# Optimization experiments

Measured on AMD Instinct MI355X. Metric: run time of the kernel, lower is better.

The kernel has to match this reference:

```python
import jax, jax.numpy as jnp
import numpy as np
from jax import lax

EMBED = 512
HID = 512
CLASSES = 3
TP, TH, B = 256, 256, 128
IN_DIM = 768


def _gru_cell(x, h, Wih, Whh, bih, bhh):
    # PyTorch GRU cell math. x: [B, in], h: [B, d]
    gi = x @ Wih.T + bih
    gh = h @ Whh.T + bhh
    i_r, i_z, i_n = jnp.split(gi, 3, axis=-1)
    h_r, h_z, h_n = jnp.split(gh, 3, axis=-1)
    r = jax.nn.sigmoid(i_r + h_r)
    z = jax.nn.sigmoid(i_z + h_z)
    n = jnp.tanh(i_n + r * h_n)
    return (1.0 - z) * n + z * h


def _gru_scan(x, h0, Wih, Whh, bih, bhh):
    # x: [T, B, in]; returns outputs [T, B, d]
    def step(h, xt):
        h = _gru_cell(xt, h, Wih, Whh, bih, bhh)
        return h, h
    _, o = lax.scan(step, h0, x)
    return o


def setup_inputs() -> dict:
    key = jax.random.key(0)
    ks = jax.random.split(key, 32)
    s = 0.02
    d = {
        'encoded_p': jax.random.normal(ks[0], (TP, B, IN_DIM), jnp.float32),
        'encoded_h': jax.random.normal(ks[1], (TH, B, IN_DIM), jnp.float32),
        'p_W': jax.random.normal(ks[2], (EMBED, IN_DIM), jnp.float32) * s,
        'p_b': jnp.zeros((EMBED,), jnp.float32),
        'h_W': jax.random.normal(ks[3], (EMBED, IN_DIM), jnp.float32) * s,
        'h_b': jnp.zeros((EMBED,), jnp.float32),
        'pg_Wih': jax.random.normal(ks[4], (3 * HID, EMBED), jnp.float32) * s,
        'pg_Whh': jax.random.normal(ks[5], (3 * HID, HID), jnp.float32) * s,
        'pg_bih': jnp.zeros((3 * HID,), jnp.float32),
        'pg_bhh': jnp.zeros((3 * HID,), jnp.float32),
        'hg_Wih': jax.random.normal(ks[6], (3 * HID, EMBED), jnp.float32) * s,
        'hg_Whh': jax.random.normal(ks[7], (3 * HID, HID), jnp.float32) * s,
        'hg_bih': jnp.zeros((3 * HID,), jnp.float32),
        'hg_bhh': jnp.zeros((3 * HID,), jnp.float32),
        'W_s': jax.random.normal(ks[8], (HID, HID), jnp.float32) * s,
        'W_t': jax.random.normal(ks[9], (HID, HID), jnp.float32) * s,
        'w_e': jax.random.normal(ks[10], (HID, 1), jnp.float32) * s,
        'W_m': jax.random.normal(ks[11], (HID, HID), jnp.float32) * s,
        'm_Wih': jax.random.normal(ks[12], (3 * HID, 2 * HID), jnp.float32) * s,
        'm_Whh': jax.random.normal(ks[13], (3 * HID, HID), jnp.float32) * s,
        'm_bih': jnp.zeros((3 * HID,), jnp.float32),
        'm_bhh': jnp.zeros((3 * HID,), jnp.float32),
        'out_W': jax.random.normal(ks[14], (CLASSES, HID), jnp.float32) * s,
        'out_b': jnp.zeros((CLASSES,), jnp.float32),
        'training': 0,
    }
    return d


def reference(encoded_p, encoded_h, p_W, p_b, h_W, h_b,
              pg_Wih, pg_Whh, pg_bih, pg_bhh,
              hg_Wih, hg_Whh, hg_bih, hg_bhh,
              W_s, W_t, w_e, W_m,
              m_Wih, m_Whh, m_bih, m_bhh,
              out_W, out_b, training):
    batch = encoded_p.shape[1]
    # dropout is identity when training is falsy (reference uses training=0)
    xp = encoded_p @ p_W.T + p_b          # [Tp, B, embed]
    xh = encoded_h @ h_W.T + h_b          # [Th, B, embed]
    h0 = jnp.ones((batch, HID), xp.dtype)  # torch.ones init hidden
    o_p = _gru_scan(xp, h0, pg_Wih, pg_Whh, pg_bih, pg_bhh)  # [Tp, B, d]
    o_h = _gru_scan(xh, h0, hg_Wih, hg_Whh, hg_bih, hg_bhh)  # [Th, B, d]

    Whs = jnp.einsum('tbd,de->tbe', o_p, W_s)  # precompute, fixed across steps
    we = w_e[:, 0]

    def step(h_m, h_t):
        Wht = h_t @ W_t                        # [B, d]
        Wm = h_m @ W_m                         # [B, d]
        M = jnp.tanh(Whs + (Wht + Wm)[None])   # [Tp, B, d]
        logits = jnp.einsum('tbd,d->bt', M, we)  # [B, Tp]
        alpha = jax.nn.softmax(logits, axis=1)
        a_t = jnp.einsum('bt,tbd->bd', alpha, o_p)
        m_t = jnp.concatenate([a_t, h_t], axis=-1)  # [B, 2d]
        h_m = _gru_cell(m_t, h_m, m_Wih, m_Whh, m_bih, m_bhh)
        return h_m, alpha

    h_m0 = jnp.ones((batch, HID), xp.dtype)
    h_star, _alphas = lax.scan(step, h_m0, o_h)
    out = h_star @ out_W.T + out_b
    out = jax.nn.relu(out)  # LAST_NON_LINEAR = True
    return out
```

## Files before the change

kernel.cpp:

```cpp
#include <hip/hip_runtime.h>
#include <cstddef>

#define TSEQ 256
#define NB   128
#define HID  512
#define G3   1536
#define INDIM 768
#define CH   16
#define NWG  256
#define FLS  32

typedef unsigned short bfraw;
using short8 = __attribute__((ext_vector_type(8))) short;
using f32x4  = __attribute__((ext_vector_type(4))) float;

#define MFMA16 __builtin_amdgcn_mfma_f32_16x16x32_bf16

__device__ __forceinline__ float bf2f(unsigned int u){ return __uint_as_float(u<<16); }
__device__ __forceinline__ bfraw f2bf(float f){
  unsigned int u = __float_as_uint(f);
  u += 0x7fffu + ((u>>16)&1u);
  return (bfraw)(u>>16);
}
__device__ __forceinline__ float fsig(float x){
  return __builtin_amdgcn_rcpf(1.0f + __expf(-x));
}
__device__ __forceinline__ float ftanh(float x){
  return 1.0f - 2.0f*__builtin_amdgcn_rcpf(1.0f + __expf(2.0f*x));
}

__device__ __forceinline__ uint4 bpu4(const void* p){
  unsigned long long a = __hip_atomic_load((const unsigned long long*)p,     __ATOMIC_RELAXED, __HIP_MEMORY_SCOPE_AGENT);
  unsigned long long b = __hip_atomic_load((const unsigned long long*)p + 1, __ATOMIC_RELAXED, __HIP_MEMORY_SCOPE_AGENT);
  uint4 r; r.x=(unsigned)a; r.y=(unsigned)(a>>32); r.z=(unsigned)b; r.w=(unsigned)(b>>32);
  return r;
}
__device__ __forceinline__ short8 bps8(const void* p){
  union{ uint4 u; short8 s; } cv; cv.u = bpu4(p); return cv.s;
}
__device__ __forceinline__ float4 bpf4(const void* p){
  union{ uint4 u; float4 f; } cv; cv.u = bpu4(p); return cv.f;
}
__device__ __forceinline__ float bpf(const void* p){
  unsigned u = __hip_atomic_load((const unsigned*)p, __ATOMIC_RELAXED, __HIP_MEMORY_SCOPE_AGENT);
  return __uint_as_float(u);
}
__device__ __forceinline__ void st4_cp(void* p, unsigned v){
  __hip_atomic_store((unsigned*)p, v, __ATOMIC_RELAXED, __HIP_MEMORY_SCOPE_AGENT);
}
__device__ __forceinline__ void st8_cp(void* p, unsigned long long v){
  __hip_atomic_store((unsigned long long*)p, v, __ATOMIC_RELAXED, __HIP_MEMORY_SCOPE_AGENT);
}
__device__ __forceinline__ void stf_cp(float* p, float v){
  __hip_atomic_store((unsigned*)p, __float_as_uint(v), __ATOMIC_RELAXED, __HIP_MEMORY_SCOPE_AGENT);
}
__device__ __forceinline__ void sth_cp(bfraw* p, bfraw v){
  __hip_atomic_store((unsigned short*)p, v, __ATOMIC_RELAXED, __HIP_MEMORY_SCOPE_AGENT);
}
__device__ __forceinline__ unsigned long long pk64(float a, float b){
  return (unsigned long long)__float_as_uint(a) | ((unsigned long long)__float_as_uint(b)<<32);
}

__device__ __forceinline__ void spin_ge(unsigned* p, unsigned epoch){
  int sp = 0;
  while (__hip_atomic_load(p, __ATOMIC_RELAXED, __HIP_MEMORY_SCOPE_AGENT) < epoch){
    if (sp < 3){ __builtin_amdgcn_s_sleep(1); ++sp; }
    else        __builtin_amdgcn_s_sleep(16);
  }
}
__device__ __forceinline__ void pollN(unsigned* flags, int n, unsigned epoch){
  const int tid = threadIdx.x;
  if (tid < n) spin_ge(&flags[tid*FLS], epoch);
  __syncthreads();
}
__device__ __forceinline__ void setflag(unsigned* f, unsigned v){
  if (threadIdx.x == 0){
    asm volatile("s_waitcnt vmcnt(0)" ::: "memory");
    __hip_atomic_store(f, v, __ATOMIC_RELAXED, __HIP_MEMORY_SCOPE_AGENT);
  }
}

__global__ void init_k(unsigned* bar){
  int i = blockIdx.x*256 + threadIdx.x;
  if (i < 4*NWG*FLS) bar[i] = 0u;
}

__global__ void hminit_k(float* hmbuf, bfraw* hm_bf){
  int i = blockIdx.x*256 + threadIdx.x;
  hmbuf[i] = 1.0f;
  hm_bf[i] = (bfraw)0x3f80;
}

__global__ __launch_bounds__(256)
void tconv_k(const float* __restrict__ in, bfraw* __restrict__ out, int R, int Cc){
  __shared__ float t[32][33];
  int c0 = blockIdx.x*32, r0 = blockIdx.y*32;
  int tx = threadIdx.x&31, ty = threadIdx.x>>5;
  #pragma unroll
  for (int i=0;i<32;i+=8) t[ty+i][tx] = in[(size_t)(r0+ty+i)*Cc + c0+tx];
  __syncthreads();
  #pragma unroll
  for (int i=0;i<32;i+=8) out[(size_t)(c0+ty+i)*R + r0+tx] = f2bf(t[tx][ty+i]);
}

__global__ void cvt_k(const float* __restrict__ in, bfraw* __restrict__ out, int n){
  int i = (blockIdx.x*256 + threadIdx.x)*4;
  if (i >= n) return;
  float4 v = *(const float4*)(in+i);
  uint2 o;
  o.x = (unsigned)f2bf(v.x) | ((unsigned)f2bf(v.y)<<16);
  o.y = (unsigned)f2bf(v.z) | ((unsigned)f2bf(v.w)<<16);
  *(uint2*)(out+i) = o;
}

__global__ void wcat_k(const float* __restrict__ mWih, const float* __restrict__ mWhh,
                       bfraw* __restrict__ Wcat){
  size_t gid = (size_t)blockIdx.x*256 + threadIdx.x;
  int np = (int)(gid / 384);
  int k4 = ((int)(gid % 384))*4;
  int dd = np>>2, g = np&3;
  float v[4];
  #pragma unroll
  for (int j=0;j<4;++j){
    int k = k4+j; float x = 0.f;
    if (g==0)      x = (k<1024) ? mWih[(size_t)dd*1024 + k]        : mWhh[(size_t)dd*512 + (k-1024)];
    else if (g==1) x = (k<1024) ? mWih[(size_t)(512+dd)*1024 + k]  : mWhh[(size_t)(512+dd)*512 + (k-1024)];
    else if (g==2) x = (k<1024) ? mWih[(size_t)(1024+dd)*1024 + k] : 0.f;
    else           x = (k<1024) ? 0.f : mWhh[(size_t)(1024+dd)*512 + (k-1024)];
    v[j] = x;
  }
  uint2 o;
  o.x = (unsigned)f2bf(v[0]) | ((unsigned)f2bf(v[1])<<16);
  o.y = (unsigned)f2bf(v[2]) | ((unsigned)f2bf(v[3])<<16);
  *(uint2*)(Wcat + (size_t)np*1536 + k4) = o;
}

__global__ void bpack_k(const float* __restrict__ mbih, const float* __restrict__ mbhh,
                        float* __restrict__ bc){
  int dd = blockIdx.x*256 + threadIdx.x;
  if (dd >= 512) return;
  bc[dd]      = mbih[dd] + mbhh[dd];
  bc[512+dd]  = mbih[512+dd] + mbhh[512+dd];
  bc[1024+dd] = mbih[1024+dd];
  bc[1536+dd] = mbhh[1024+dd];
}

__global__ void fuse_bias_k(const float* __restrict__ Wih, const float* __restrict__ bih,
                            const float* __restrict__ pb, float* __restrict__ bout)
{
  int g = blockIdx.x*256 + threadIdx.x;
  if (g >= G3) return;
  float acc = bih[g];
  const float* w = Wih + (size_t)g*HID;
  for (int e=0;e<HID;e+=4){
    float4 wv = *(const float4*)(w+e);
    float4 pv = *(const float4*)(pb+e);
    acc += wv.x*pv.x + wv.y*pv.y + wv.z*pv.z + wv.w*pv.w;
  }
  bout[g] = acc;
}

template<typename TA, typename TC, bool BIAS>
__global__ __launch_bounds__(256)
void mgemm(const TA* __restrict__ A0, const TA* __restrict__ A1,
           const bfraw* __restrict__ B0, const bfraw* __restrict__ B1,
           const float* __restrict__ bias0, const float* __restrict__ bias1,
           TC* __restrict__ C0, TC* __restrict__ C1,
           int K, int lda, int ldb, int ldc)
{
  const TA* A = blockIdx.z ? A1 : A0;
  const bfraw* B = blockIdx.z ? B1 : B0;
  const float* bias = blockIdx.z ? bias1 : bias0;
  TC* C = blockIdx.z ? C1 : C0;
  __shared__ bfraw Al[128*40];
  __shared__ bfraw Bl[128*40];
  const int tid = threadIdx.x;
  const size_t m0 = (size_t)blockIdx.y*128, n0 = (size_t)blockIdx.x*128;
  const int w = tid>>6, l = tid&63;
  const int wr = (w>>1)*64, wc = (w&1)*64;
  const int fr = l&15, fg = l>>4;
  f32x4 acc[4][4];
  #pragma unroll
  for (int i=0;i<4;++i)
    #pragma unroll
    for (int j=0;j<4;++j) acc[i][j] = (f32x4){0.f,0.f,0.f,0.f};

  const int srow = tid>>1, skc = (tid&1)*16;
  for (int k0=0; k0<K; k0+=32){
    if constexpr (sizeof(TA)==4){
      const float* ap = (const float*)A + (m0+srow)*lda + k0 + skc;
      float4 v0=*(const float4*)ap, v1=*(const float4*)(ap+4),
             v2=*(const float4*)(ap+8), v3=*(const float4*)(ap+12);
      uint4 w0, w1;
      w0.x=(unsigned)f2bf(v0.x)|((unsigned)f2bf(v0.y)<<16);
      w0.y=(unsigned)f2bf(v0.z)|((unsigned)f2bf(v0.w)<<16);
      w0.z=(unsigned)f2bf(v1.x)|((unsigned)f2bf(v1.y)<<16);
      w0.w=(unsigned)f2bf(v1.z)|((unsigned)f2bf(v1.w)<<16);
      w1.x=(unsigned)f2bf(v2.x)|((unsigned)f2bf(v2.y)<<16);
      w1.y=(unsigned)f2bf(v2.z)|((unsigned)f2bf(v2.w)<<16);
      w1.z=(unsigned)f2bf(v3.x)|((unsigned)f2bf(v3.y)<<16);
      w1.w=(unsigned)f2bf(v3.z)|((unsigned)f2bf(v3.w)<<16);
      *(uint4*)&Al[srow*40+skc]   = w0;
      *(uint4*)&Al[srow*40+skc+8] = w1;
    } else {
      const bfraw* ap = (const bfraw*)A + (m0+srow)*lda + k0 + skc;
      *(uint4*)&Al[srow*40+skc]   = *(const uint4*)ap;
      *(uint4*)&Al[srow*40+skc+8] = *(const uint4*)(ap+8);
    }
    {
      const bfraw* bp = B + (n0+srow)*ldb + k0 + skc;
      *(uint4*)&Bl[srow*40+skc]   = *(const uint4*)bp;
      *(uint4*)&Bl[srow*40+skc+8] = *(const uint4*)(bp+8);
    }
    __syncthreads();
    short8 af[4], bfr[4];
    #pragma unroll
    for (int i=0;i<4;++i) af[i]  = *(const short8*)&Al[(wr+i*16+fr)*40 + fg*8];
    #pragma unroll
    for (int j=0;j<4;++j) bfr[j] = *(const short8*)&Bl[(wc+j*16+fr)*40 + fg*8];
    #pragma unroll
    for (int i=0;i<4;++i)
      #pragma unroll
      for (int j=0;j<4;++j)
        acc[i][j] = MFMA16(af[i], bfr[j], acc[i][j], 0,0,0);
    __syncthreads();
  }
  #pragma unroll
  for (int i=0;i<4;++i){
    #pragma unroll
    for (int j=0;j<4;++j){
      size_t n = n0 + wc + j*16 + fr;
      float bv = BIAS ? bias[n] : 0.f;
      #pragma unroll
      for (int r=0;r<4;++r){
        size_t m = m0 + wr + i*16 + fg*4 + r;
        float v = acc[i][j][r] + bv;
        if constexpr (sizeof(TC)==2) ((bfraw*)C)[m*ldc + n] = f2bf(v);
        else                         ((float*)C)[m*ldc + n] = v;
      }
    }
  }
}

__global__ __launch_bounds__(512, 2)
void scanB(const float* __restrict__ GIp, const float* __restrict__ GIh,
           const bfraw* __restrict__ Whhp, const bfraw* __restrict__ Whhh,
           const float* __restrict__ bhhp, const float* __restrict__ bhhh,
           float* __restrict__ hst, bfraw* __restrict__ o_p, bfraw* __restrict__ o_h,
           int c0, unsigned* __restrict__ bar)
{
  extern __shared__ char smem[];
  bfraw* wl = (bfraw*)smem;
  float* sh = (float*)(smem + 98304);
  const int wg = blockIdx.x;
  const int z = wg>>7, rem = wg&127;
  const int bg = rem>>4, dg = rem&15;
  const float* GI  = z ? GIh : GIp;
  const bfraw* Wb  = z ? Whhh : Whhp;
  const float* bhh = z ? bhhh : bhhp;
  bfraw* ob = z ? o_h : o_p;
  float* hz = hst + (size_t)z*2*NB*HID;
  const int tid = threadIdx.x;
  unsigned* bfl = bar + 3*NWG*FLS;
  unsigned* grp = bfl + (size_t)(z*128 + bg*16)*FLS;
  unsigned* own = bfl + (size_t)wg*FLS;

  #pragma unroll
  for (int g=0; g<3; ++g){
    const unsigned* src = (const unsigned*)(Wb + (size_t)(g*512 + dg*32)*512);
    for (int j=0; j<16; ++j){
      int iu = tid + j*512;
      unsigned v = src[iu];
      int d = iu>>8, kk = (iu&255)*2;
      int idx0 = g*16384 + (kk>>2)*128 + d*4 + (kk&3);
      *((unsigned*)wl + (idx0>>1)) = v;
    }
  }
  __syncthreads();

  const int bl = tid>>5, dl = tid&31;
  const int d = dg*32+dl, bglob = bg*16+bl;
  const float br = bhh[d], bz = bhh[512+d], bn = bhh[1024+d];

  #pragma clang loop unroll(disable)
  for (int tt=0; tt<CH; ++tt){
    const int t = c0+tt;
    if (t > 0) pollN(grp, 16, (unsigned)t);
    if (t == 0){
      for (int j=0;j<4;++j){
        int i4 = tid + j*512;
        *(float4*)&sh[i4*4] = (float4){1.f,1.f,1.f,1.f};
      }
    } else {
      const float* hp = hz + (size_t)((t-1)&1)*NB*HID + (size_t)bg*16*HID;
      for (int j=0;j<4;++j){
        int i4 = tid + j*512;
        *(float4*)&sh[i4*4] = bpf4(&hp[i4*4]);
      }
    }
    __syncthreads();
    float ar = br, az = bz, an = bn;
    const float* hb = sh + bl*512;
    for (int k=0;k<512;k+=4){
      float4 h4 = *(const float4*)(hb+k);
      int base = (k>>2)*128 + dl*4;
      uint2 wr = *(const uint2*)(wl + base);
      uint2 wz = *(const uint2*)(wl + 16384 + base);
      uint2 wn = *(const uint2*)(wl + 32768 + base);
      ar += h4.x*bf2f(wr.x&0xffffu) + h4.y*bf2f(wr.x>>16) + h4.z*bf2f(wr.y&0xffffu) + h4.w*bf2f(wr.y>>16);
      az += h4.x*bf2f(wz.x&0xffffu) + h4.y*bf2f(wz.x>>16) + h4.z*bf2f(wz.y&0xffffu) + h4.w*bf2f(wz.y>>16);
      an += h4.x*bf2f(wn.x&0xffffu) + h4.y*bf2f(wn.x>>16) + h4.z*bf2f(wn.y&0xffffu) + h4.w*bf2f(wn.y>>16);
    }
    const float* gi = GI + ((size_t)tt*NB + bglob)*G3;
    float r  = fsig(gi[d] + ar);
    float zz = fsig(gi[512+d] + az);
    float n  = ftanh(gi[1024+d] + r*an);
    float hp = hb[d];
    float hv = (1.0f-zz)*n + zz*hp;
    stf_cp(&(hz + (size_t)(t&1)*NB*HID)[(size_t)bglob*HID + d], hv);
    ob[((size_t)t*NB + bglob)*HID + d] = f2bf(hv);
    __syncthreads();
    setflag(own, (unsigned)(t+1));
  }
}

__global__ __launch_bounds__(512, 2)
void scanD(const bfraw* __restrict__ Whs, const bfraw* __restrict__ o_p,
           const bfraw* __restrict__ o_h,
           const bfraw* __restrict__ WtT, const bfraw* __restrict__ WmT,
           const float* __restrict__ w_e,
           const bfraw* __restrict__ Wcat, const float* __restrict__ bc,
           float* __restrict__ hmbuf, bfraw* __restrict__ hm_bf,
           bfraw* __restrict__ a_bf, float* __restrict__ Lbuf, float* __restrict__ Gx,
           const float* __restrict__ outW, const float* __restrict__ outb,
           float* __restrict__ out, unsigned* __restrict__ bar)
{
  extern __shared__ char smem[];
  bfraw* whs_l = (bfraw*)smem;
  float* pt    = (float*)(smem + 131072);
  float* xlf   = (float*)(smem + 147456);
  float* hml   = (float*)(smem + 149504);
  float* c_l   = (float*)(smem + 151552);
  float* lp0   = (float*)(smem + 152576);
  float* lp1   = (float*)(smem + 153600);
  float* l_s   = (float*)(smem + 154624);
  float* red   = (float*)(smem + 155648);

  const int wg = blockIdx.x, tid = threadIdx.x;
  const int b = wg>>1, dh = wg&1;
  unsigned* pf  = bar;
  unsigned* afl = bar + NWG*FLS;
  unsigned* hfl = bar + 2*NWG*FLS;

  for (int it=0; it<16; ++it){
    int idx = tid + it*512;
    int tq = idx>>5, c = idx&31;
    const bfraw* src = Whs + ((size_t)tq*NB + b)*HID + dh*256 + c*8;
    *(uint4*)&whs_l[tq*256 + ((c ^ (tq&15))<<3)] = *(const uint4*)src;
  }
  const int cc_ = tid&31;
  float we8[8];
  #pragma unroll
  for (int r=0;r<8;++r) we8[r] = w_e[dh*256 + cc_*8 + r];
  __syncthreads();

  const int gs = wg&127, gbgrp = gs>>4, gddg = gs&15;
  const int gw = tid>>6, gl = tid&63, gfr = gl&15, gfg = gl>>4;
  const int n0w = gddg*128 + gw*16;
  const int mb0 = gbgrp*16;
  const bfraw* wrowA = Wcat + (size_t)(n0w+gfr)*1536;

  #pragma clang loop unroll(disable)
  for (int t=0; t<TSEQ; ++t){
    const int rs = (t+1)&1;
    const bfraw* hmr = hm_bf + (size_t)rs*65536;
    const float* hpr = hmbuf + (size_t)rs*65536;
    bfraw* hmw = hm_bf + (size_t)(t&1)*65536;
    float* hpw = hmbuf + (size_t)(t&1)*65536;

    if (t > 0){
      if (tid < 16) spin_ge(&hfl[((b>>4)*16 + tid)*FLS], (unsigned)t);
      else if (wg < 128 && tid < 32) spin_ge(&hfl[(gbgrp*16 + (tid-16))*FLS], (unsigned)t);
      else if (wg >= 128 && tid == 16) spin_ge(&hfl[gs*FLS], (unsigned)t);
      __syncthreads();
    }

    if (tid < 64){
      uint4 u = *(const uint4*)(o_h + ((size_t)t*NB + b)*HID + tid*8);
      float4 f0, f1;
      f0.x=bf2f(u.x&0xffffu); f0.y=bf2f(u.x>>16); f0.z=bf2f(u.y&0xffffu); f0.w=bf2f(u.y>>16);
      f1.x=bf2f(u.z&0xffffu); f1.y=bf2f(u.z>>16); f1.z=bf2f(u.w&0xffffu); f1.w=bf2f(u.w>>16);
      *(float4*)&xlf[tid*8]   = f0;
      *(float4*)&xlf[tid*8+4] = f1;
    } else if (tid < 192){
      int i2 = tid - 64;
      *(float4*)&hml[i2*4] = bpf4(hpr + (size_t)b*HID + i2*4);
    }
    __syncthreads();

    {
      const int el = tid>>1, kh = tid&1;
      const bfraw* wt = WtT + (size_t)(dh*256+el)*HID + kh*256;
      const bfraw* wm = WmT + (size_t)(dh*256+el)*HID + kh*256;
      const float* xv = xlf + kh*256;
      const float* hv = hml + kh*256;
      float acc = 0.f;
      #pragma unroll 4
      for (int k8=0;k8<32;++k8){
        uint4 wu = *(const uint4*)(wt+k8*8);
        uint4 mu = *(const uint4*)(wm+k8*8);
        float4 x0 = *(const float4*)(xv+k8*8), x1 = *(const float4*)(xv+k8*8+4);
        float4 h0 = *(const float4*)(hv+k8*8), h1 = *(const float4*)(hv+k8*8+4);
        acc += x0.x*bf2f(wu.x&0xffffu) + x0.y*bf2f(wu.x>>16) + x0.z*bf2f(wu.y&0xffffu) + x0.w*bf2f(wu.y>>16);
        acc += x1.x*bf2f(wu.z&0xffffu) + x1.y*bf2f(wu.z>>16) + x1.z*bf2f(wu.w&0xffffu) + x1.w*bf2f(wu.w>>16);
        acc += h0.x*bf2f(mu.x&0xffffu) + h0.y*bf2f(mu.x>>16) + h0.z*bf2f(mu.y&0xffffu) + h0.w*bf2f(mu.y>>16);
        acc += h1.x*bf2f(mu.z&0xffffu) + h1.y*bf2f(mu.z>>16) + h1.z*bf2f(mu.w&0xffffu) + h1.w*bf2f(mu.w>>16);
      }
      acc += __shfl_xor(acc, 1);
      if (kh == 0) c_l[el] = acc;
    }
    __syncthreads();

    {
      const int tqs = tid>>5;
      float c8[8];
      *(float4*)&c8[0] = *(const float4*)&c_l[cc_*8];
      *(float4*)&c8[4] = *(const float4*)&c_l[cc_*8+4];
      #pragma unroll 2
      for (int i=0;i<16;++i){
        int tq = tqs + i*16;
        uint4 u = *(const uint4*)&whs_l[tq*256 + ((cc_ ^ (tq&15))<<3)];
        float s = 0.f;
        #pragma unroll
        for (int j=0;j<4;++j){
          unsigned uu = ((const unsigned*)&u)[j];
          s += ftanh(bf2f(uu&0xffffu) + c8[j*2])   * we8[j*2];
          s += ftanh(bf2f(uu>>16)     + c8[j*2+1]) * we8[j*2+1];
        }
        #pragma unroll
        for (int off=16; off; off>>=1) s += __shfl_xor(s, off);
        if (cc_ == 0) lp0[tq] = s;
      }
    }
    __syncthreads();
    if (tid < 64){
      float4 v = *(const float4*)&lp0[tid*4];
      st8_cp(&Lbuf[(size_t)wg*256 + tid*4],     pk64(v.x, v.y));
      st8_cp(&Lbuf[(size_t)wg*256 + tid*4 + 2], pk64(v.z, v.w));
    }
    __syncthreads();
    setflag(&pf[wg*FLS], (unsigned)(t+1));

    const int dgrp = tid&31, tqs2 = tid>>5, d8 = dgrp*8;
    const bfraw* opb = o_p + (size_t)b*HID + dh*256 + d8;
    uint4 uu[16];
    #pragma unroll
    for (int i=0;i<16;++i)
      uu[i] = *(const uint4*)(opb + (size_t)(tqs2*16 + i)*NB*HID);

    f32x4 accA = {0.f,0.f,0.f,0.f};
    if (wg < 128){
      const bfraw* hrow = hmr + (size_t)(mb0+gfr)*HID;
      #pragma unroll
      for (int kk=0; kk<16; ++kk){
        short8 af = bps8(hrow + kk*32 + gfg*8);
        short8 bv = *(const short8*)(wrowA + 1024 + kk*32 + gfg*8);
        accA = MFMA16(af, bv, accA, 0,0,0);
      }
    } else {
      f32x4 accB = {0.f,0.f,0.f,0.f};
      const bfraw* xrow = o_h + ((size_t)t*NB + mb0+gfr)*HID;
      #pragma unroll
      for (int kk=0; kk<16; ++kk){
        short8 af = *(const short8*)(xrow + kk*32 + gfg*8);
        short8 bv = *(const short8*)(wrowA + 512 + kk*32 + gfg*8);
        accB = MFMA16(af, bv, accB, 0,0,0);
      }
      #pragma unroll
      for (int rr=0; rr<4; ++rr)
        stf_cp(&Gx[(size_t)(mb0 + gfg*4 + rr)*2048 + n0w + gfr], accB[rr]);
    }

    if (tid == 0) spin_ge(&pf[(wg^1)*FLS], (unsigned)(t+1));
    __syncthreads();
    if (tid < 64) *(float4*)&lp1[tid*4] = bpf4(&Lbuf[(size_t)(wg^1)*256 + tid*4]);
    __syncthreads();

    {
      const int lane = tid&63;
      float v = -1e30f, e = 0.f;
      if (tid < TSEQ){
        v = lp0[tid] + lp1[tid];
        float m = v;
        #pragma unroll
        for (int off=32; off; off>>=1) m = fmaxf(m, __shfl_xor(m, off));
        if (lane==0) red[tid>>6] = m;
      }
      __syncthreads();
      float mx = fmaxf(fmaxf(red[0],red[1]), fmaxf(red[2],red[3]));
      if (tid < TSEQ){
        e = __expf(v - mx);
        float s2 = e;
        #pragma unroll
        for (int off=32; off; off>>=1) s2 += __shfl_xor(s2, off);
        if (lane==0) red[8+(tid>>6)] = s2;
      }
      __syncthreads();
      float S = red[8]+red[9]+red[10]+red[11];
      if (tid < TSEQ) l_s[tid] = e * __builtin_amdgcn_rcpf(S);
      __syncthreads();
    }

    {
      float a0=0,a1=0,a2=0,a3=0,a4=0,a5=0,a6=0,a7=0;
      #pragma unroll
      for (int i=0;i<16;++i){
        float al = l_s[tqs2*16 + i];
        uint4 u = uu[i];
        a0 += al*bf2f(u.x&0xffffu); a1 += al*bf2f(u.x>>16);
        a2 += al*bf2f(u.y&0xffffu); a3 += al*bf2f(u.y>>16);
        a4 += al*bf2f(u.z&0xffffu); a5 += al*bf2f(u.z>>16);
        a6 += al*bf2f(u.w&0xffffu); a7 += al*bf2f(u.w>>16);
      }
      *(float4*)&pt[tqs2*256+d8]   = (float4){a0,a1,a2,a3};
      *(float4*)&pt[tqs2*256+d8+4] = (float4){a4,a5,a6,a7};
      __syncthreads();
      if (tid < 256){
        float sA = 0.f;
        #pragma unroll
        for (int ss=0;ss<16;++ss) sA += pt[ss*256 + tid];
        float sB = __shfl_down(sA, 1);
        if ((tid&1)==0){
          unsigned pk = (unsigned)f2bf(sA) | ((unsigned)f2bf(sB)<<16);
          st4_cp(a_bf + (size_t)b*HID + dh*256 + tid, pk);
        }
      }
    }
    __syncthreads();
    setflag(&afl[wg*FLS], (unsigned)(t+1));

    if (wg < 128){
      if (tid < 32) spin_ge(&afl[(gbgrp*32 + tid)*FLS], (unsigned)(t+1));
      else if (tid == 32) spin_ge(&afl[(128 + gs)*FLS], (unsigned)(t+1));
      __syncthreads();

      const bfraw* arow = a_bf + (size_t)(mb0+gfr)*HID;
      #pragma unroll
      for (int kk=0; kk<16; ++kk){
        short8 af = bps8(arow + kk*32 + gfg*8);
        short8 bv = *(const short8*)(wrowA + kk*32 + gfg*8);
        accA = MFMA16(af, bv, accA, 0,0,0);
      }
      const int np = n0w + gfr, dd = np>>2, g = np&3;
      #pragma unroll
      for (int rr=0; rr<4; ++rr){
        float x0 = accA[rr] + bpf(&Gx[(size_t)(mb0 + gfg*4 + rr)*2048 + np]);
        float x1 = __shfl_xor(x0, 1);
        float x2 = __shfl_xor(x0, 2);
        float x3 = __shfl_xor(x1, 2);
        if (g==0){
          int b3 = mb0 + gfg*4 + rr;
          float hp = bpf(&hpr[(size_t)b3*HID + dd]);
          float rg = fsig(x0 + bc[dd]);
          float zg = fsig(x1 + bc[512+dd]);
          float gn = ftanh(x2 + bc[1024+dd] + rg*(x3 + bc[1536+dd]));
          float h = (1.f-zg)*gn + zg*hp;
          stf_cp(&hpw[(size_t)b3*HID + dd], h);
          sth_cp(&hmw[(size_t)b3*HID + dd], f2bf(h));
        }
      }
      __syncthreads();
      setflag(&hfl[wg*FLS], (unsigned)(t+1));
    }
  }

  if (wg == 0){
    pollN(hfl, 128, (unsigned)TSEQ);
    if (tid < NB*3){
      const float* hf = hmbuf + (size_t)((TSEQ-1)&1)*65536;
      int b2 = tid/3, c = tid%3;
      float acc = outb[c];
      const float* h = hf + (size_t)b2*HID;
      const float* w = outW + (size_t)c*HID;
      for (int d2=0; d2<HID; ++d2) acc = fmaf(bpf(h+d2), w[d2], acc);
      out[tid] = fmaxf(acc, 0.f);
    }
  }
}

extern "C" void kernel_launch(void* const* d_in, const int* in_sizes, int n_in,
                              void* d_out, int out_size, void* d_ws, size_t ws_size,
                              hipStream_t stream)
{
  const float* Ep    = (const float*)d_in[0];
  const float* Eh    = (const float*)d_in[1];
  const float* p_W   = (const float*)d_in[2];
  const float* p_b   = (const float*)d_in[3];
  const float* h_W   = (const float*)d_in[4];
  const float* h_b   = (const float*)d_in[5];
  const float* pgWih = (const float*)d_in[6];
  const float* pgWhh = (const float*)d_in[7];
  const float* pgbih = (const float*)d_in[8];
  const float* pgbhh = (const float*)d_in[9];
  const float* hgWih = (const float*)d_in[10];
  const float* hgWhh = (const float*)d_in[11];
  const float* hgbih = (const float*)d_in[12];
  const float* hgbhh = (const float*)d_in[13];
  const float* W_s   = (const float*)d_in[14];
  const float* W_t   = (const float*)d_in[15];
  const float* w_e   = (const float*)d_in[16];
  const float* W_m   = (const float*)d_in[17];
  const float* mWih  = (const float*)d_in[18];
  const float* mWhh  = (const float*)d_in[19];
  const float* mbih  = (const float*)d_in[20];
  const float* mbhh  = (const float*)d_in[21];
  const float* outW  = (const float*)d_in[22];
  const float* outb  = (const float*)d_in[23];

  const size_t OB    = (size_t)TSEQ*NB*HID*sizeof(bfraw);
  const size_t RB    = OB;
  const size_t WFB   = (size_t)G3*INDIM*sizeof(bfraw);
  const size_t SQB   = (size_t)HID*HID*sizeof(bfraw);
  const size_t WHHB  = (size_t)G3*HID*sizeof(bfraw);
  const size_t WCATB = (size_t)2048*1536*sizeof(bfraw);
  const size_t BARB  = (size_t)4*NWG*FLS*sizeof(unsigned);
  const size_t needed = 2*OB + RB + 2*WFB + 3*SQB + 2*WHHB + WCATB
                        + 8192 + 2*6144
                        + 4*262144 + 2*262144 + 2*131072
                        + BARB;
  if (ws_size < needed) return;

  char* p = (char*)d_ws;
  bfraw* o_p_bf = (bfraw*)p; p += OB;
  bfraw* o_h_bf = (bfraw*)p; p += OB;
  char*  Rreg   = p;         p += RB;
  bfraw* Wfp_bf = (bfraw*)p; p += WFB;
  bfraw* Wfh_bf = (bfraw*)p; p += WFB;
  bfraw* WsT_bf = (bfraw*)p; p += SQB;
  bfraw* WtT_bf = (bfraw*)p; p += SQB;
  bfraw* WmT_bf = (bfraw*)p; p += SQB;
  bfraw* Whhp_bf= (bfraw*)p; p += WHHB;
  bfraw* Whhh_bf= (bfraw*)p; p += WHHB;
  bfraw* Wcat_bf= (bfraw*)p; p += WCATB;
  float* bc     = (float*)p; p += 8192;
  float* bfp    = (float*)p; p += 6144;
  float* bfh    = (float*)p; p += 6144;
  float* hst    = (float*)p; p += 4*262144;
  float* hmbuf  = (float*)p; p += 2*262144;
  bfraw* hm_bf  = (bfraw*)p; p += 2*131072;
  unsigned* bar = (unsigned*)p; p += BARB;

  bfraw* pWT_bf = (bfraw*)Rreg;
  bfraw* hWT_bf = (bfraw*)(Rreg + (size_t)INDIM*HID*sizeof(bfraw));
  float* GIp_c  = (float*)Rreg;
  float* GIh_c  = (float*)(Rreg + (size_t)CH*NB*G3*sizeof(float));
  bfraw* Whs_bf = (bfraw*)Rreg;
  float* Lbuf   = (float*)Wfp_bf;
  bfraw* a_bf   = (bfraw*)((char*)Wfp_bf + 2097152);
  float* Gx     = (float*)((char*)Wfp_bf + WFB);

  (void)hipFuncSetAttribute((const void*)scanB, hipFuncAttributeMaxDynamicSharedMemorySize, 131072);
  (void)hipFuncSetAttribute((const void*)scanD, hipFuncAttributeMaxDynamicSharedMemorySize, 155776);

  dim3 b256(256), b512(512);

  init_k<<<dim3(128), b256, 0, stream>>>(bar);
  hminit_k<<<dim3(512), b256, 0, stream>>>(hmbuf, hm_bf);

  tconv_k<<<dim3(INDIM/32, HID/32), b256, 0, stream>>>(p_W, pWT_bf, HID, INDIM);
  tconv_k<<<dim3(INDIM/32, HID/32), b256, 0, stream>>>(h_W, hWT_bf, HID, INDIM);
  tconv_k<<<dim3(HID/32, HID/32),  b256, 0, stream>>>(W_s, WsT_bf, HID, HID);
  tconv_k<<<dim3(HID/32, HID/32),  b256, 0, stream>>>(W_t, WtT_bf, HID, HID);
  tconv_k<<<dim3(HID/32, HID/32),  b256, 0, stream>>>(W_m, WmT_bf, HID, HID);
  cvt_k<<<dim3((G3*HID)/1024), b256, 0, stream>>>(pgWhh, Whhp_bf, G3*HID);
  cvt_k<<<dim3((G3*HID)/1024), b256, 0, stream>>>(hgWhh, Whhh_bf, G3*HID);
  wcat_k<<<dim3(3072), b256, 0, stream>>>(mWih, mWhh, Wcat_bf);
  bpack_k<<<dim3(2), b256, 0, stream>>>(mbih, mbhh, bc);
  fuse_bias_k<<<dim3(G3/256), b256, 0, stream>>>(pgWih, pgbih, p_b, bfp);
  fuse_bias_k<<<dim3(G3/256), b256, 0, stream>>>(hgWih, hgbih, h_b, bfh);
  mgemm<float, bfraw, false><<<dim3(INDIM/128, G3/128, 2), b256, 0, stream>>>(
    pgWih, hgWih, pWT_bf, hWT_bf, nullptr, nullptr, Wfp_bf, Wfh_bf,
    HID, HID, HID, INDIM);

  for (int c = 0; c < TSEQ/CH; ++c){
    mgemm<float, float, true><<<dim3(G3/128, (CH*NB)/128, 2), b256, 0, stream>>>(
      Ep + (size_t)c*CH*NB*INDIM, Eh + (size_t)c*CH*NB*INDIM,
      Wfp_bf, Wfh_bf, bfp, bfh, GIp_c, GIh_c,
      INDIM, INDIM, INDIM, G3);
    scanB<<<dim3(NWG), b512, 131072, stream>>>(
      GIp_c, GIh_c, Whhp_bf, Whhh_bf, pgbhh, hgbhh,
      hst, o_p_bf, o_h_bf, c*CH, bar);
  }

  mgemm<bfraw, bfraw, false><<<dim3(HID/128, (TSEQ*NB)/128, 1), b256, 0, stream>>>(
    o_p_bf, o_p_bf, WsT_bf, WsT_bf, nullptr, nullptr, Whs_bf, Whs_bf,
    HID, HID, HID, HID);

  scanD<<<dim3(NWG), b512, 155776, stream>>>(
    Whs_bf, o_p_bf, o_h_bf, WtT_bf, WmT_bf, w_e, Wcat_bf, bc,
    hmbuf, hm_bf, a_bf, Lbuf, Gx,
    outW, outb, (float*)d_out, bar);
}
```

Baseline: 18.66 ms.

## Split attention over time halves and drop per-step logits exchange

Reassigns the scanD workgroup pair from splitting the hidden dimension to splitting the time dimension, so each workgroup computes complete logits for its 128 timesteps without exchanging partial logits with its partner. Softmax is made unnormalised (no max subtraction): each half publishes an exp-weighted context and exp-sum, which the GRU workgroups combine and normalise. The x-side gate MFMA is folded into the GRU workgroups, removing the Gx buffer and its flag wait. This removes a cross-workgroup handshake per step, at the cost of possible exp overflow for large logits and more compute per GRU workgroup.

```diff
diff --git a/kernel.cpp b/kernel.cpp
--- a/kernel.cpp
+++ b/kernel.cpp
@@ -48,17 +48,11 @@
 __device__ __forceinline__ void st4_cp(void* p, unsigned v){
   __hip_atomic_store((unsigned*)p, v, __ATOMIC_RELAXED, __HIP_MEMORY_SCOPE_AGENT);
 }
-__device__ __forceinline__ void st8_cp(void* p, unsigned long long v){
-  __hip_atomic_store((unsigned long long*)p, v, __ATOMIC_RELAXED, __HIP_MEMORY_SCOPE_AGENT);
-}
 __device__ __forceinline__ void stf_cp(float* p, float v){
   __hip_atomic_store((unsigned*)p, __float_as_uint(v), __ATOMIC_RELAXED, __HIP_MEMORY_SCOPE_AGENT);
 }
 __device__ __forceinline__ void sth_cp(bfraw* p, bfraw v){
   __hip_atomic_store((unsigned short*)p, v, __ATOMIC_RELAXED, __HIP_MEMORY_SCOPE_AGENT);
-}
-__device__ __forceinline__ unsigned long long pk64(float a, float b){
-  return (unsigned long long)__float_as_uint(a) | ((unsigned long long)__float_as_uint(b)<<32);
 }
 
 __device__ __forceinline__ void spin_ge(unsigned* p, unsigned epoch){
@@ -324,47 +318,45 @@
   }
 }
 
-__global__ __launch_bounds__(512, 2)
+__global__ __launch_bounds__(512, 1)
 void scanD(const bfraw* __restrict__ Whs, const bfraw* __restrict__ o_p,
            const bfraw* __restrict__ o_h,
            const bfraw* __restrict__ WtT, const bfraw* __restrict__ WmT,
            const float* __restrict__ w_e,
            const bfraw* __restrict__ Wcat, const float* __restrict__ bc,
            float* __restrict__ hmbuf, bfraw* __restrict__ hm_bf,
-           bfraw* __restrict__ a_bf, float* __restrict__ Lbuf, float* __restrict__ Gx,
+           bfraw* __restrict__ aU, float* __restrict__ Sbuf,
            const float* __restrict__ outW, const float* __restrict__ outb,
            float* __restrict__ out, unsigned* __restrict__ bar)
 {
   extern __shared__ char smem[];
   bfraw* whs_l = (bfraw*)smem;
   float* pt    = (float*)(smem + 131072);
-  float* xlf   = (float*)(smem + 147456);
-  float* hml   = (float*)(smem + 149504);
-  float* c_l   = (float*)(smem + 151552);
-  float* lp0   = (float*)(smem + 152576);
-  float* lp1   = (float*)(smem + 153600);
-  float* l_s   = (float*)(smem + 154624);
-  float* red   = (float*)(smem + 155648);
+  bfraw* a_l   = (bfraw*)(smem + 131072);
+  float* xlf   = (float*)(smem + 147712);
+  float* hml   = (float*)(smem + 149760);
+  float* c_l   = (float*)(smem + 151808);
+  float* l_s   = (float*)(smem + 153856);
+  float* red   = (float*)(smem + 154368);
 
   const int wg = blockIdx.x, tid = threadIdx.x;
-  const int b = wg>>1, dh = wg&1;
-  unsigned* pf  = bar;
+  const int b = wg>>1, th = wg&1;
   unsigned* afl = bar + NWG*FLS;
   unsigned* hfl = bar + 2*NWG*FLS;
 
   for (int it=0; it<16; ++it){
     int idx = tid + it*512;
-    int tq = idx>>5, c = idx&31;
-    const bfraw* src = Whs + ((size_t)tq*NB + b)*HID + dh*256 + c*8;
-    *(uint4*)&whs_l[tq*256 + ((c ^ (tq&15))<<3)] = *(const uint4*)src;
+    int row = idx>>6, c = idx&63;
+    const bfraw* src = Whs + ((size_t)(th*128+row)*NB + b)*HID + c*8;
+    *(uint4*)&whs_l[row*512 + ((c ^ ((row&31)<<1))<<3)] = *(const uint4*)src;
   }
   const int cc_ = tid&31;
-  float we8[8];
+  float we16[16];
   #pragma unroll
-  for (int r=0;r<8;++r) we8[r] = w_e[dh*256 + cc_*8 + r];
+  for (int r=0;r<16;++r) we16[r] = w_e[cc_*16 + r];
   __syncthreads();
 
-  const int gs = wg&127, gbgrp = gs>>4, gddg = gs&15;
+  const int gbgrp = wg>>4, gddg = wg&15;
   const int gw = tid>>6, gl = tid&63, gfr = gl&15, gfg = gl>>4;
   const int n0w = gddg*128 + gw*16;
   const int mb0 = gbgrp*16;
@@ -380,8 +372,6 @@
 
     if (t > 0){
       if (tid < 16) spin_ge(&hfl[((b>>4)*16 + tid)*FLS], (unsigned)t);
-      else if (wg < 128 && tid < 32) spin_ge(&hfl[(gbgrp*16 + (tid-16))*FLS], (unsigned)t);
-      else if (wg >= 128 && tid == 16) spin_ge(&hfl[gs*FLS], (unsigned)t);
       __syncthreads();
     }
 
@@ -399,162 +389,150 @@
     __syncthreads();
 
     {
-      const int el = tid>>1, kh = tid&1;
-      const bfraw* wt = WtT + (size_t)(dh*256+el)*HID + kh*256;
-      const bfraw* wm = WmT + (size_t)(dh*256+el)*HID + kh*256;
-      const float* xv = xlf + kh*256;
-      const float* hv = hml + kh*256;
+      const bfraw* wt = WtT + (size_t)tid*HID;
+      const bfraw* wm = WmT + (size_t)tid*HID;
       float acc = 0.f;
       #pragma unroll 4
-      for (int k8=0;k8<32;++k8){
+      for (int k8=0;k8<64;++k8){
         uint4 wu = *(const uint4*)(wt+k8*8);
         uint4 mu = *(const uint4*)(wm+k8*8);
-        float4 x0 = *(const float4*)(xv+k8*8), x1 = *(const float4*)(xv+k8*8+4);
-        float4 h0 = *(const float4*)(hv+k8*8), h1 = *(const float4*)(hv+k8*8+4);
+        float4 x0 = *(const float4*)(xlf+k8*8), x1 = *(const float4*)(xlf+k8*8+4);
+        float4 h0 = *(const float4*)(hml+k8*8), h1 = *(const float4*)(hml+k8*8+4);
         acc += x0.x*bf2f(wu.x&0xffffu) + x0.y*bf2f(wu.x>>16) + x0.z*bf2f(wu.y&0xffffu) + x0.w*bf2f(wu.y>>16);
         acc += x1.x*bf2f(wu.z&0xffffu) + x1.y*bf2f(wu.z>>16) + x1.z*bf2f(wu.w&0xffffu) + x1.w*bf2f(wu.w>>16);
         acc += h0.x*bf2f(mu.x&0xffffu) + h0.y*bf2f(mu.x>>16) + h0.z*bf2f(mu.y&0xffffu) + h0.w*bf2f(mu.y>>16);
         acc += h1.x*bf2f(mu.z&0xffffu) + h1.y*bf2f(mu.z>>16) + h1.z*bf2f(mu.w&0xffffu) + h1.w*bf2f(mu.w>>16);
       }
-      acc += __shfl_xor(acc, 1);
-      if (kh == 0) c_l[el] = acc;
+      c_l[tid] = acc;
     }
     __syncthreads();
 
     {
       const int tqs = tid>>5;
-      float c8[8];
-      *(float4*)&c8[0] = *(const float4*)&c_l[cc_*8];
-      *(float4*)&c8[4] = *(const float4*)&c_l[cc_*8+4];
+      float c16[16];
+      *(float4*)&c16[0]  = *(const float4*)&c_l[cc_*16];
+      *(float4*)&c16[4]  = *(const float4*)&c_l[cc_*16+4];
+      *(float4*)&c16[8]  = *(const float4*)&c_l[cc_*16+8];
+      *(float4*)&c16[12] = *(const float4*)&c_l[cc_*16+12];
       #pragma unroll 2
-      for (int i=0;i<16;++i){
-        int tq = tqs + i*16;
-        uint4 u = *(const uint4*)&whs_l[tq*256 + ((cc_ ^ (tq&15))<<3)];
+      for (int i=0;i<8;++i){
+        int row = tqs*8 + i;
+        int swz = (row&31)<<1;
+        uint4 u0 = *(const uint4*)&whs_l[row*512 + (((2*cc_)   ^ swz)<<3)];
+        uint4 u1 = *(const uint4*)&whs_l[row*512 + (((2*cc_+1) ^ swz)<<3)];
         float s = 0.f;
         #pragma unroll
         for (int j=0;j<4;++j){
-          unsigned uu = ((const unsigned*)&u)[j];
-          s += ftanh(bf2f(uu&0xffffu) + c8[j*2])   * we8[j*2];
-          s += ftanh(bf2f(uu>>16)     + c8[j*2+1]) * we8[j*2+1];
+          unsigned a = ((const unsigned*)&u0)[j];
+          s += ftanh(bf2f(a&0xffffu) + c16[j*2])   * we16[j*2];
+          s += ftanh(bf2f(a>>16)     + c16[j*2+1]) * we16[j*2+1];
+        }
+        #pragma unroll
+        for (int j=0;j<4;++j){
+          unsigned a = ((const unsigned*)&u1)[j];
+          s += ftanh(bf2f(a&0xffffu) + c16[8+j*2])   * we16[8+j*2];
+          s += ftanh(bf2f(a>>16)     + c16[8+j*2+1]) * we16[8+j*2+1];
         }
         #pragma unroll
         for (int off=16; off; off>>=1) s += __shfl_xor(s, off);
-        if (cc_ == 0) lp0[tq] = s;
-      }
-    }
-    __syncthreads();
-    if (tid < 64){
-      float4 v = *(const float4*)&lp0[tid*4];
-      st8_cp(&Lbuf[(size_t)wg*256 + tid*4],     pk64(v.x, v.y));
-      st8_cp(&Lbuf[(size_t)wg*256 + tid*4 + 2], pk64(v.z, v.w));
-    }
-    __syncthreads();
-    setflag(&pf[wg*FLS], (unsigned)(t+1));
-
-    const int dgrp = tid&31, tqs2 = tid>>5, d8 = dgrp*8;
-    const bfraw* opb = o_p + (size_t)b*HID + dh*256 + d8;
-    uint4 uu[16];
-    #pragma unroll
-    for (int i=0;i<16;++i)
-      uu[i] = *(const uint4*)(opb + (size_t)(tqs2*16 + i)*NB*HID);
-
-    f32x4 accA = {0.f,0.f,0.f,0.f};
-    if (wg < 128){
-      const bfraw* hrow = hmr + (size_t)(mb0+gfr)*HID;
-      #pragma unroll
-      for (int kk=0; kk<16; ++kk){
-        short8 af = bps8(hrow + kk*32 + gfg*8);
-        short8 bv = *(const short8*)(wrowA + 1024 + kk*32 + gfg*8);
-        accA = MFMA16(af, bv, accA, 0,0,0);
-      }
-    } else {
-      f32x4 accB = {0.f,0.f,0.f,0.f};
-      const bfraw* xrow = o_h + ((size_t)t*NB + mb0+gfr)*HID;
-      #pragma unroll
-      for (int kk=0; kk<16; ++kk){
-        short8 af = *(const short8*)(xrow + kk*32 + gfg*8);
-        short8 bv = *(const short8*)(wrowA + 512 + kk*32 + gfg*8);
-        accB = MFMA16(af, bv, accB, 0,0,0);
-      }
-      #pragma unroll
-      for (int rr=0; rr<4; ++rr)
-        stf_cp(&Gx[(size_t)(mb0 + gfg*4 + rr)*2048 + n0w + gfr], accB[rr]);
-    }
-
-    if (tid == 0) spin_ge(&pf[(wg^1)*FLS], (unsigned)(t+1));
-    __syncthreads();
-    if (tid < 64) *(float4*)&lp1[tid*4] = bpf4(&Lbuf[(size_t)(wg^1)*256 + tid*4]);
+        if (cc_ == 0) l_s[row] = s;
+      }
+    }
     __syncthreads();
 
     {
-      const int lane = tid&63;
-      float v = -1e30f, e = 0.f;
-      if (tid < TSEQ){
-        v = lp0[tid] + lp1[tid];
-        float m = v;
+      float eS = 0.f;
+      if (tid < 128){
+        float e = __expf(l_s[tid]);
+        l_s[tid] = e;
+        eS = e;
         #pragma unroll
-        for (int off=32; off; off>>=1) m = fmaxf(m, __shfl_xor(m, off));
-        if (lane==0) red[tid>>6] = m;
-      }
-      __syncthreads();
-      float mx = fmaxf(fmaxf(red[0],red[1]), fmaxf(red[2],red[3]));
-      if (tid < TSEQ){
-        e = __expf(v - mx);
-        float s2 = e;
-        #pragma unroll
-        for (int off=32; off; off>>=1) s2 += __shfl_xor(s2, off);
-        if (lane==0) red[8+(tid>>6)] = s2;
-      }
-      __syncthreads();
-      float S = red[8]+red[9]+red[10]+red[11];
-      if (tid < TSEQ) l_s[tid] = e * __builtin_amdgcn_rcpf(S);
-      __syncthreads();
-    }
+        for (int off=32; off; off>>=1) eS += __shfl_xor(eS, off);
+        if ((tid&63)==0) red[tid>>6] = eS;
+      }
+    }
+    __syncthreads();
 
     {
+      const int g8 = tid>>6, dgrp = tid&63, d8 = dgrp*8;
+      const bfraw* opb = o_p + (size_t)b*HID + d8;
+      uint4 uu[16];
+      #pragma unroll
+      for (int i=0;i<16;++i)
+        uu[i] = *(const uint4*)(opb + (size_t)(th*128 + g8*16 + i)*NB*HID);
       float a0=0,a1=0,a2=0,a3=0,a4=0,a5=0,a6=0,a7=0;
       #pragma unroll
       for (int i=0;i<16;++i){
-        float al = l_s[tqs2*16 + i];
+        float al = l_s[g8*16 + i];
         uint4 u = uu[i];
         a0 += al*bf2f(u.x&0xffffu); a1 += al*bf2f(u.x>>16);
         a2 += al*bf2f(u.y&0xffffu); a3 += al*bf2f(u.y>>16);
         a4 += al*bf2f(u.z&0xffffu); a5 += al*bf2f(u.z>>16);
         a6 += al*bf2f(u.w&0xffffu); a7 += al*bf2f(u.w>>16);
       }
-      *(float4*)&pt[tqs2*256+d8]   = (float4){a0,a1,a2,a3};
-      *(float4*)&pt[tqs2*256+d8+4] = (float4){a4,a5,a6,a7};
+      *(float4*)&pt[g8*512+d8]   = (float4){a0,a1,a2,a3};
+      *(float4*)&pt[g8*512+d8+4] = (float4){a4,a5,a6,a7};
       __syncthreads();
-      if (tid < 256){
-        float sA = 0.f;
+      float sA = 0.f;
+      #pragma unroll
+      for (int ss=0;ss<8;++ss) sA += pt[ss*512 + tid];
+      float sB = __shfl_down(sA, 1);
+      if (!(tid&1)){
+        unsigned pk = (unsigned)f2bf(sA) | ((unsigned)f2bf(sB)<<16);
+        st4_cp(aU + ((size_t)th*NB + b)*HID + tid, pk);
+      }
+      if (tid == 0) stf_cp(&Sbuf[wg*FLS], red[0] + red[1]);
+    }
+    __syncthreads();
+    setflag(&afl[wg*FLS], (unsigned)(t+1));
+
+    if (wg < 128){
+      f32x4 accA = {0.f,0.f,0.f,0.f};
+      const bfraw* hrow = hmr + (size_t)(mb0+gfr)*HID;
+      const bfraw* xrow = o_h + ((size_t)t*NB + mb0+gfr)*HID;
+      #pragma unroll
+      for (int kk=0; kk<16; ++kk){
+        short8 af = bps8(hrow + kk*32 + gfg*8);
+        short8 bv = *(const short8*)(wrowA + 1024 + kk*32 + gfg*8);
+        accA = MFMA16(af, bv, accA, 0,0,0);
+      }
+      #pragma unroll
+      for (int kk=0; kk<16; ++kk){
+        short8 af = *(const short8*)(xrow + kk*32 + gfg*8);
+        short8 bv = *(const short8*)(wrowA + 512 + kk*32 + gfg*8);
+        accA = MFMA16(af, bv, accA, 0,0,0);
+      }
+      if (tid < 32) spin_ge(&afl[(gbgrp*32 + tid)*FLS], (unsigned)(t+1));
+      __syncthreads();
+      {
+        const int rb = tid>>5, seg = tid&31, d0 = seg*16;
+        const bfraw* p0 = aU + (size_t)(mb0+rb)*HID + d0;
+        const bfraw* p1 = aU + (size_t)(NB + mb0+rb)*HID + d0;
+        float S = bpf(&Sbuf[(2*(mb0+rb))*FLS]) + bpf(&Sbuf[(2*(mb0+rb)+1)*FLS]);
+        float rn = __builtin_amdgcn_rcpf(S);
+        short8 a0a = bps8(p0), a0b = bps8(p0+8);
+        short8 a1a = bps8(p1), a1b = bps8(p1+8);
         #pragma unroll
-        for (int ss=0;ss<16;++ss) sA += pt[ss*256 + tid];
-        float sB = __shfl_down(sA, 1);
-        if ((tid&1)==0){
-          unsigned pk = (unsigned)f2bf(sA) | ((unsigned)f2bf(sB)<<16);
-          st4_cp(a_bf + (size_t)b*HID + dh*256 + tid, pk);
+        for (int j=0;j<4;++j){
+          float f0 = (bf2f((unsigned short)a0a[j*2])   + bf2f((unsigned short)a1a[j*2]))   * rn;
+          float f1 = (bf2f((unsigned short)a0a[j*2+1]) + bf2f((unsigned short)a1a[j*2+1])) * rn;
+          *(unsigned*)&a_l[rb*520 + d0 + j*2] = (unsigned)f2bf(f0) | ((unsigned)f2bf(f1)<<16);
+          float g0 = (bf2f((unsigned short)a0b[j*2])   + bf2f((unsigned short)a1b[j*2]))   * rn;
+          float g1 = (bf2f((unsigned short)a0b[j*2+1]) + bf2f((unsigned short)a1b[j*2+1])) * rn;
+          *(unsigned*)&a_l[rb*520 + d0 + 8 + j*2] = (unsigned)f2bf(g0) | ((unsigned)f2bf(g1)<<16);
         }
       }
-    }
-    __syncthreads();
-    setflag(&afl[wg*FLS], (unsigned)(t+1));
-
-    if (wg < 128){
-      if (tid < 32) spin_ge(&afl[(gbgrp*32 + tid)*FLS], (unsigned)(t+1));
-      else if (tid == 32) spin_ge(&afl[(128 + gs)*FLS], (unsigned)(t+1));
       __syncthreads();
-
-      const bfraw* arow = a_bf + (size_t)(mb0+gfr)*HID;
       #pragma unroll
       for (int kk=0; kk<16; ++kk){
-        short8 af = bps8(arow + kk*32 + gfg*8);
+        short8 af = *(const short8*)&a_l[gfr*520 + kk*32 + gfg*8];
         short8 bv = *(const short8*)(wrowA + kk*32 + gfg*8);
         accA = MFMA16(af, bv, accA, 0,0,0);
       }
       const int np = n0w + gfr, dd = np>>2, g = np&3;
       #pragma unroll
       for (int rr=0; rr<4; ++rr){
-        float x0 = accA[rr] + bpf(&Gx[(size_t)(mb0 + gfg*4 + rr)*2048 + np]);
+        float x0 = accA[rr];
         float x1 = __shfl_xor(x0, 1);
         float x2 = __shfl_xor(x0, 2);
         float x3 = __shfl_xor(x1, 2);
@@ -655,12 +633,11 @@
   float* GIp_c  = (float*)Rreg;
   float* GIh_c  = (float*)(Rreg + (size_t)CH*NB*G3*sizeof(float));
   bfraw* Whs_bf = (bfraw*)Rreg;
-  float* Lbuf   = (float*)Wfp_bf;
-  bfraw* a_bf   = (bfraw*)((char*)Wfp_bf + 2097152);
-  float* Gx     = (float*)((char*)Wfp_bf + WFB);
+  bfraw* aU     = (bfraw*)Wfp_bf;
+  float* Sbuf   = (float*)((char*)Wfp_bf + 262144);
 
   (void)hipFuncSetAttribute((const void*)scanB, hipFuncAttributeMaxDynamicSharedMemorySize, 131072);
-  (void)hipFuncSetAttribute((const void*)scanD, hipFuncAttributeMaxDynamicSharedMemorySize, 155776);
+  (void)hipFuncSetAttribute((const void*)scanD, hipFuncAttributeMaxDynamicSharedMemorySize, 154496);
 
   dim3 b256(256), b512(512);
 
@@ -696,8 +673,8 @@
     o_p_bf, o_p_bf, WsT_bf, WsT_bf, nullptr, nullptr, Whs_bf, Whs_bf,
     HID, HID, HID, HID);
 
-  scanD<<<dim3(NWG), b512, 155776, stream>>>(
+  scanD<<<dim3(NWG), b512, 154496, stream>>>(
     Whs_bf, o_p_bf, o_h_bf, WtT_bf, WmT_bf, w_e, Wcat_bf, bc,
-    hmbuf, hm_bf, a_bf, Lbuf, Gx,
+    hmbuf, hm_bf, aU, Sbuf,
     outW, outb, (float*)d_out, bar);
 }
```

New measurement: 21.13 ms. +13.2%, slower.
